# Kernel tuning notes

Measured on AMD Instinct MI355X. Metric: run time of the kernel, lower is better.

## Reference

```python
import jax, jax.numpy as jnp
import numpy as np

SLIDING_WINDOW = 512  # matches init kwarg
BLOCK_STRIDE = 32     # tokens per cache page


def setup_inputs() -> dict:
    key = jax.random.key(0)
    k0, k1, k2, k3 = jax.random.split(key, 4)
    B, S, HQ, HKV, D = 2, 2048, 32, 8, 128
    nb = S // BLOCK_STRIDE
    q = jax.random.normal(k0, (B, S, HQ, D), jnp.float32)
    k = jax.random.normal(k1, (B, S, HKV, D), jnp.float32)
    v = jax.random.normal(k2, (B, S, HKV, D), jnp.float32)
    sink = jax.random.normal(k3, (HQ,), jnp.float32)
    cache_state = jnp.zeros((B * nb, 2, HKV, BLOCK_STRIDE, D), jnp.float32)
    seq_block_ids = jnp.arange(B * nb, dtype=jnp.int32).reshape(B, nb)
    return {"q": q, "k": k, "v": v, "cache_state": cache_state,
            "seq_block_ids": seq_block_ids, "sink": sink}


def reference(q, k, v, cache_state, seq_block_ids, sink):
    B, S, HQ, D = q.shape
    HKV = k.shape[2]
    G = HQ // HKV  # GQA group size
    stride = cache_state.shape[3]
    nb = S // stride

    # --- write prefill K/V into the paged cache ---
    # pages laid out [num_pages, k/v, HKV, stride, D]
    k_pg = k.reshape(B, nb, stride, HKV, D).transpose(0, 1, 3, 2, 4).reshape(B * nb, HKV, stride, D)
    v_pg = v.reshape(B, nb, stride, HKV, D).transpose(0, 1, 3, 2, 4).reshape(B * nb, HKV, stride, D)
    ids = seq_block_ids.reshape(-1)
    new_cache = cache_state.at[ids, 0].set(k_pg).at[ids, 1].set(v_pg)

    # --- sliding-window causal attention with sink logits (GQA, no repeat) ---
    scale = 1.0 / np.sqrt(D).astype(np.float32)
    qg = q.reshape(B, S, HKV, G, D)
    # scores: [B, HKV, G, Sq, Sk]
    scores = jnp.einsum('bqhgd,bshd->bhgqs', qg, k) * scale
    i = jnp.arange(S)[:, None]
    j = jnp.arange(S)[None, :]
    allowed = (j <= i) & ((i - j) < SLIDING_WINDOW)  # causal banded mask
    neg = jnp.finfo(scores.dtype).min
    scores = jnp.where(allowed, scores, neg)
    # per-head sink logit appended as extra key column, dropped after softmax
    sink_col = jnp.broadcast_to(sink.reshape(HKV, G)[None, :, :, None, None], (B, HKV, G, S, 1))
    probs = jax.nn.softmax(jnp.concatenate([scores, sink_col], axis=-1), axis=-1)[..., :S]
    out = jnp.einsum('bhgqs,bshd->bqhgd', probs, v).reshape(B, S, HQ, D)
    return out, new_cache
```

## Files before the change

kernel.cpp:

```cpp
#include <hip/hip_runtime.h>
#include <hip/hip_bf16.h>
#include <stdint.h>

#define BB 2
#define SS 2048
#define HQ 32
#define HKV 8
#define DD 128
#define WIN 512

typedef __bf16 bf16x8 __attribute__((ext_vector_type(8)));
typedef float f32x16 __attribute__((ext_vector_type(16)));

__device__ __forceinline__ bf16x8 cvt8(float4 a, float4 b, float s) {
  bf16x8 r;
  r[0] = (__bf16)(a.x * s); r[1] = (__bf16)(a.y * s);
  r[2] = (__bf16)(a.z * s); r[3] = (__bf16)(a.w * s);
  r[4] = (__bf16)(b.x * s); r[5] = (__bf16)(b.y * s);
  r[6] = (__bf16)(b.z * s); r[7] = (__bf16)(b.w * s);
  return r;
}

__device__ __forceinline__ uint32_t pk2(float lo, float hi) {
  uint32_t w;
  asm("v_cvt_pk_bf16_f32 %0, %1, %2" : "=v"(w) : "v"(lo), "v"(hi));
  return w;
}

__global__ __launch_bounds__(512, 2) void attn_kernel(
    const float* __restrict__ qg, const float* __restrict__ kg,
    const float* __restrict__ vg, const float* __restrict__ sinkg,
    float* __restrict__ outg)
{
  const int col = (blockIdx.x & 7) + 8 * ((blockIdx.x >> 3) & 1);
  const int rank = blockIdx.x >> 4;
  const int qtile = rank < 24 ? rank + 8 : 31 - rank;
  const int hkv = col & 7, b = col >> 3;
  const int qb = qtile * 64;
  const int tid = threadIdx.x;
  const int wave = tid >> 6, lane = tid & 63;
  const int c5 = lane & 31, hi = lane >> 5;
  const int hq = (hkv << 2) + (wave >> 1);
  const int qw = qb + (wave & 1) * 32;
  const int qrow = qw + c5;

  __shared__ __align__(16) __bf16 Kl[2][64 * 128];
  __shared__ __align__(16) __bf16 Vt[2][128 * 64];

  const float LOG2E = 1.4426950408889634f;
  const float scale = 0.08838834764831845f * LOG2E;
  const float THR = 12.0f;

  bf16x8 qf[8];
  {
    const float* qp = qg + (((size_t)b * SS + qrow) * HQ + hq) * DD + hi * 8;
    #pragma unroll
    for (int ch = 0; ch < 8; ++ch) {
      float4 a = *(const float4*)(qp + ch * 16);
      float4 a2 = *(const float4*)(qp + ch * 16 + 4);
      qf[ch] = cvt8(a, a2, scale);
    }
  }
  const float sk = sinkg[hq] * LOG2E;

  float mm = -1e30f, ll = 0.f;
  f32x16 acc[4];
  #pragma unroll
  for (int d = 0; d < 4; ++d)
    #pragma unroll
    for (int r = 0; r < 16; ++r) acc[d][r] = 0.f;

  const int t0 = (qb > (WIN - 1) ? (qb - (WIN - 1)) : 0) >> 6;
  const int t1 = (qb + 63) >> 6;

  const int krow = tid >> 3, kchunk = tid & 7;
  const int vd = tid & 127, vslot = tid >> 7;
  const size_t KSTEP = (size_t)64 * HKV * DD;
  const float* kBase = kg + (((size_t)b * SS + krow) * HKV + hkv) * DD + kchunk * 16;
  const float* vBase = vg + (((size_t)b * SS + vslot * 16) * HKV + hkv) * DD + vd;

  float4 k0, k1, k2, k3; float vr[16];
  auto issue = [&](int t) {
    const float* kp = kBase + (size_t)t * KSTEP;
    k0 = *(const float4*)(kp);     k1 = *(const float4*)(kp + 4);
    k2 = *(const float4*)(kp + 8); k3 = *(const float4*)(kp + 12);
    const float* vp = vBase + (size_t)t * KSTEP;
    #pragma unroll
    for (int j = 0; j < 16; ++j) vr[j] = vp[(size_t)j * (HKV * DD)];
  };
  const int ksw = ((krow ^ (krow >> 3)) & 7) << 4;
  const int vsw = ((vd ^ (vd >> 3)) & 7) << 4;
  auto commit = [&](int buf) {
    char* kd = (char*)(&Kl[buf][0]) + krow * 256;
    *(bf16x8*)(kd + ((kchunk * 32) ^ ksw)) = cvt8(k0, k1, 1.f);
    *(bf16x8*)(kd + ((kchunk * 32 + 16) ^ ksw)) = cvt8(k2, k3, 1.f);
    char* vdst = (char*)(&Vt[buf][0]) + vd * 128;
    bf16x8 w0, w1;
    #pragma unroll
    for (int j = 0; j < 8; ++j) { w0[j] = (__bf16)vr[j]; w1[j] = (__bf16)vr[8 + j]; }
    *(bf16x8*)(vdst + ((vslot * 32) ^ vsw)) = w0;
    *(bf16x8*)(vdst + ((vslot * 32 + 16) ^ vsw)) = w1;
  };

  issue(t0);
  commit(0);
  __syncthreads();
  int cur = 0;

  const int swA = ((c5 ^ (c5 >> 3)) & 7) << 4;
  const int swB = swA ^ 0x40;

  for (int t = t0; t <= t1; ++t) {
    if (t < t1) issue(t + 1);
    const int kb = t << 6;
    const char* Ksc = (const char*)&Kl[cur][0];
    const char* Vsc = (const char*)&Vt[cur][0];

    f32x16 s0, s1;
    #pragma unroll
    for (int r = 0; r < 16; ++r) { s0[r] = 0.f; s1[r] = 0.f; }
    __builtin_amdgcn_s_setprio(1);
    #pragma unroll
    for (int ch = 0; ch < 8; ++ch) {
      const int colb = ch * 32 + hi * 16;
      bf16x8 a0 = *(const bf16x8*)(Ksc + c5 * 256 + (colb ^ swA));
      bf16x8 a1 = *(const bf16x8*)(Ksc + (32 + c5) * 256 + (colb ^ swB));
      s0 = __builtin_amdgcn_mfma_f32_32x32x16_bf16(a0, qf[ch], s0, 0, 0, 0);
      s1 = __builtin_amdgcn_mfma_f32_32x32x16_bf16(a1, qf[ch], s1, 0, 0, 0);
    }
    __builtin_amdgcn_s_setprio(0);

    const bool noMask = (kb + 63 <= qw) && (kb >= qw - (WIN - 32));

    if (!noMask) {
      #pragma unroll
      for (int r = 0; r < 16; ++r) {
        const int lr = (r & 3) + 8 * (r >> 2) + 4 * hi;
        const int kv0 = kb + lr, kv1 = kv0 + 32;
        const bool ok0 = (kv0 <= qrow) && (qrow - kv0 < WIN);
        const bool ok1 = (kv1 <= qrow) && (qrow - kv1 < WIN);
        s0[r] = ok0 ? s0[r] : -1e30f;
        s1[r] = ok1 ? s1[r] : -1e30f;
      }
    }
    float tmax = s0[0];
    #pragma unroll
    for (int r = 1; r < 16; ++r) tmax = fmaxf(tmax, s0[r]);
    #pragma unroll
    for (int r = 0; r < 16; ++r) tmax = fmaxf(tmax, s1[r]);
    tmax = fmaxf(tmax, __shfl_xor(tmax, 32));

    const bool resc = __any(tmax > mm + THR);
    const float mnew = resc ? fmaxf(mm, tmax) : mm;
    float tsum = 0.f;
    if (noMask) {
      #pragma unroll
      for (int r = 0; r < 16; ++r) {
        s0[r] = exp2f(s0[r] - mnew); tsum += s0[r];
        s1[r] = exp2f(s1[r] - mnew); tsum += s1[r];
      }
    } else {
      #pragma unroll
      for (int r = 0; r < 16; ++r) {
        s0[r] = (s0[r] > -9e29f) ? exp2f(s0[r] - mnew) : 0.f; tsum += s0[r];
        s1[r] = (s1[r] > -9e29f) ? exp2f(s1[r] - mnew) : 0.f; tsum += s1[r];
      }
    }
    tsum += __shfl_xor(tsum, 32);

    if (resc) {
      const float scl = exp2f(mm - mnew);
      ll = ll * scl + tsum;
      #pragma unroll
      for (int d = 0; d < 4; ++d)
        #pragma unroll
        for (int r = 0; r < 16; ++r) acc[d][r] *= scl;
      mm = mnew;
    } else {
      ll += tsum;
    }

    bf16x8 pb[4];
    #pragma unroll
    for (int kvq = 0; kvq < 4; ++kvq) {
      const int bq = (kvq & 1) * 8;
      float e0, e1, e2, e3, e4, e5, e6, e7;
      if (kvq & 2) {
        e0 = s1[bq+0]; e1 = s1[bq+1]; e2 = s1[bq+2]; e3 = s1[bq+3];
        e4 = s1[bq+4]; e5 = s1[bq+5]; e6 = s1[bq+6]; e7 = s1[bq+7];
      } else {
        e0 = s0[bq+0]; e1 = s0[bq+1]; e2 = s0[bq+2]; e3 = s0[bq+3];
        e4 = s0[bq+4]; e5 = s0[bq+5]; e6 = s0[bq+6]; e7 = s0[bq+7];
      }
      const uint32_t A0 = pk2(e0, e1), A1 = pk2(e2, e3);
      const uint32_t B0 = pk2(e4, e5), B1 = pk2(e6, e7);
      const uint32_t XA0 = __shfl_xor(A0, 32), XA1 = __shfl_xor(A1, 32);
      const uint32_t XB0 = __shfl_xor(B0, 32), XB1 = __shfl_xor(B1, 32);
      union { uint4 u; bf16x8 v; } cvu;
      cvu.u.x = hi ? XB0 : A0;
      cvu.u.y = hi ? XB1 : A1;
      cvu.u.z = hi ? B0 : XA0;
      cvu.u.w = hi ? B1 : XA1;
      pb[kvq] = cvu.v;
    }

    __builtin_amdgcn_s_setprio(1);
    #pragma unroll
    for (int d = 0; d < 4; ++d) {
      const int rowb = (d * 32 + c5) * 128;
      const int swV = swA ^ ((d & 1) << 6);
      #pragma unroll
      for (int kvq = 0; kvq < 4; ++kvq) {
        bf16x8 va = *(const bf16x8*)(Vsc + rowb + ((kvq * 32 + hi * 16) ^ swV));
        acc[d] = __builtin_amdgcn_mfma_f32_32x32x16_bf16(va, pb[kvq], acc[d], 0, 0, 0);
      }
    }
    __builtin_amdgcn_s_setprio(0);

    if (t < t1) {
      commit(cur ^ 1);
      __syncthreads();
      cur ^= 1;
    }
  }

  {
    const float Mf = fmaxf(mm, sk);
    const float ex = exp2f(mm - Mf);
    const float denom = ll * ex + exp2f(sk - Mf);
    const float fac = ex / denom;
    float* orow = outg + (((size_t)b * SS + qrow) * HQ + hq) * DD;
    #pragma unroll
    for (int d = 0; d < 4; ++d) {
      #pragma unroll
      for (int q4 = 0; q4 < 4; ++q4) {
        float4 o;
        o.x = acc[d][q4 * 4 + 0] * fac;
        o.y = acc[d][q4 * 4 + 1] * fac;
        o.z = acc[d][q4 * 4 + 2] * fac;
        o.w = acc[d][q4 * 4 + 3] * fac;
        *(float4*)(orow + d * 32 + q4 * 8 + 4 * hi) = o;
      }
    }
  }
}

__global__ void build_inv(const int* __restrict__ ids, int* __restrict__ inv,
                          int npages, int nslots) {
  const int i = threadIdx.x;
  if (i < npages) inv[i] = -1;
  __syncthreads();
  if (i < nslots) inv[ids[i]] = i;
}

__global__ void page_fill(const float* __restrict__ kg, const float* __restrict__ vg,
                          const float* __restrict__ cache_in, const int* __restrict__ inv,
                          float* __restrict__ cache) {
  const int page = blockIdx.x, half = blockIdx.y;
  const int slot = inv[page];
  float4* d4 = (float4*)cache;
  const size_t dbase = (((size_t)page * 2 + half) * 8) * 1024;
  if (slot >= 0) {
    const int b = slot >> 6, blk = slot & 63;
    const float4* s4 = (const float4*)(half ? vg : kg);
    for (int f = threadIdx.x; f < 8192; f += blockDim.x) {
      const int d = f & 31, s = (f >> 5) & 31, h = f >> 10;
      d4[dbase + (size_t)h * 1024 + s * 32 + d] =
          s4[(((size_t)b * SS + blk * 32 + s) * 8 + h) * 32 + d];
    }
  } else {
    const float4* s4 = (const float4*)cache_in;
    for (int f = threadIdx.x; f < 8192; f += blockDim.x)
      d4[dbase + f] = s4[dbase + f];
  }
}

__global__ void cache_copy(const float* __restrict__ src, float* __restrict__ dst, int n4) {
  const float4* s = (const float4*)src;
  float4* d = (float4*)dst;
  for (int i = blockIdx.x * blockDim.x + threadIdx.x; i < n4; i += gridDim.x * blockDim.x)
    d[i] = s[i];
}
__global__ void cache_scatter(const float* __restrict__ kg, const float* __restrict__ vg,
                              const int* __restrict__ ids, float* __restrict__ cache) {
  const int slot = blockIdx.x;
  const int half = blockIdx.y;
  const int b = slot >> 6, blk = slot & 63;
  const int page = ids[slot];
  const float4* s4 = (const float4*)(half ? vg : kg);
  float4* d4 = (float4*)cache;
  for (int f = threadIdx.x; f < 8192; f += blockDim.x) {
    const int d = f & 31, s = (f >> 5) & 31, h = f >> 10;
    d4[(((size_t)page * 2 + half) * 8 + h) * 1024 + s * 32 + d] =
        s4[(((size_t)b * SS + blk * 32 + s) * 8 + h) * 32 + d];
  }
}

extern "C" void kernel_launch(void* const* d_in, const int* in_sizes, int n_in,
                              void* d_out, int out_size, void* d_ws, size_t ws_size,
                              hipStream_t stream) {
  const float* q = (const float*)d_in[0];
  const float* k = (const float*)d_in[1];
  const float* v = (const float*)d_in[2];
  const float* cache_in = (const float*)d_in[3];
  const int* ids = (const int*)d_in[4];
  const float* sink = (const float*)d_in[5];
  float* out = (float*)d_out;
  float* cache_out = out + (size_t)BB * SS * HQ * DD;

  const int nslots = in_sizes[4];
  const int npages = in_sizes[3] / (2 * HKV * 32 * DD);

  if (ws_size >= (size_t)npages * sizeof(int) && npages <= 1024) {
    int* inv = (int*)d_ws;
    build_inv<<<1, 1024, 0, stream>>>(ids, inv, npages, nslots);
    page_fill<<<dim3(npages, 2), 256, 0, stream>>>(k, v, cache_in, inv, cache_out);
  } else {
    cache_copy<<<4096, 256, 0, stream>>>(cache_in, cache_out, (BB * SS * HKV * DD * 2) / 4);
    cache_scatter<<<dim3(BB * 64, 2), 256, 0, stream>>>(k, v, ids, cache_out);
  }
  attn_kernel<<<512, 512, 0, stream>>>(q, k, v, sink, out);
}
```

Baseline: 108.4 us.

## Precast K/V to bf16 with transposed V in workspace before attention

Adds a prep kernel that converts K to bf16 and writes a per-tile transposed bf16 V into workspace. The attention kernel then loads tiles with contiguous 16-byte vector loads and copies them straight into shared memory, replacing the strided fp32 loads and per-element conversion inside its pipelined loop. It also skips QK/PV work for 64-key tiles that lie entirely outside a wave's 32-row window. The cost is an extra kernel launch plus an extra read and write of all of K and V; the old path stays as a fallback when workspace is too small.

```diff
diff --git a/kernel.cpp b/kernel.cpp
--- a/kernel.cpp
+++ b/kernel.cpp
@@ -27,7 +27,262 @@
   return w;
 }
 
+__device__ __forceinline__ unsigned short bfu(float x) {
+  union { __bf16 b; unsigned short u; } c; c.b = (__bf16)x; return c.u;
+}
+
+#define SWZ(r) ((((r) ^ ((r) >> 3)) & 7) << 4)
+
 __global__ __launch_bounds__(512, 2) void attn_kernel(
+    const float* __restrict__ qg, const float* __restrict__ sinkg,
+    float* __restrict__ outg,
+    const unsigned short* __restrict__ kbg, const unsigned short* __restrict__ vtg)
+{
+  const int col = (blockIdx.x & 7) + 8 * ((blockIdx.x >> 3) & 1);
+  const int rank = blockIdx.x >> 4;
+  const int qtile = rank < 24 ? rank + 8 : 31 - rank;
+  const int hkv = col & 7, b = col >> 3;
+  const int qb = qtile * 64;
+  const int tid = threadIdx.x;
+  const int wave = tid >> 6, lane = tid & 63;
+  const int c5 = lane & 31, hi = lane >> 5;
+  const int hq = (hkv << 2) + (wave >> 1);
+  const int qw = qb + (wave & 1) * 32;
+  const int qrow = qw + c5;
+
+  __shared__ __align__(16) __bf16 Kl[2][64 * 128];
+  __shared__ __align__(16) __bf16 Vt[2][128 * 64];
+
+  const float LOG2E = 1.4426950408889634f;
+  const float scale = 0.08838834764831845f * LOG2E;
+  const float THR = 12.0f;
+
+  bf16x8 qf[8];
+  {
+    const float* qp = qg + (((size_t)b * SS + qrow) * HQ + hq) * DD + hi * 8;
+    #pragma unroll
+    for (int ch = 0; ch < 8; ++ch) {
+      float4 a = *(const float4*)(qp + ch * 16);
+      float4 a2 = *(const float4*)(qp + ch * 16 + 4);
+      qf[ch] = cvt8(a, a2, scale);
+    }
+  }
+  const float sk = sinkg[hq] * LOG2E;
+
+  float mm = -1e30f, ll = 0.f;
+  f32x16 acc[4];
+  #pragma unroll
+  for (int d = 0; d < 4; ++d)
+    #pragma unroll
+    for (int r = 0; r < 16; ++r) acc[d][r] = 0.f;
+
+  const int t0 = (qb > (WIN - 1) ? (qb - (WIN - 1)) : 0) >> 6;
+  const int t1 = (qb + 63) >> 6;
+
+  const char* kcol = (const char*)kbg + (size_t)(b * HKV + hkv) * (SS * DD * 2);
+  const char* vcol = (const char*)vtg + (size_t)(b * HKV + hkv) * (SS * DD * 2);
+  const int p0 = tid * 32;
+  const int kr = p0 >> 8, kx = p0 & 255;
+  const int vrw = p0 >> 7, vx = p0 & 127;
+  const int kd0 = kr * 256 + (kx ^ SWZ(kr)), kd1 = kr * 256 + ((kx + 16) ^ SWZ(kr));
+  const int vd0 = vrw * 128 + (vx ^ SWZ(vrw)), vd1 = vrw * 128 + ((vx + 16) ^ SWZ(vrw));
+
+  uint4 ksA, ksB, vsA, vsB;
+  auto issue = [&](int t) {
+    const char* kt = kcol + (size_t)t * 16384;
+    const char* vt = vcol + (size_t)t * 16384;
+    ksA = *(const uint4*)(kt + p0); ksB = *(const uint4*)(kt + p0 + 16);
+    vsA = *(const uint4*)(vt + p0); vsB = *(const uint4*)(vt + p0 + 16);
+  };
+  auto commit = [&](int buf) {
+    char* kb_ = (char*)&Kl[buf][0]; char* vb_ = (char*)&Vt[buf][0];
+    *(uint4*)(kb_ + kd0) = ksA; *(uint4*)(kb_ + kd1) = ksB;
+    *(uint4*)(vb_ + vd0) = vsA; *(uint4*)(vb_ + vd1) = vsB;
+  };
+
+  issue(t0);
+  commit(0);
+  __syncthreads();
+  int cur = 0;
+
+  const int swA = SWZ(c5);
+  const int swB = swA ^ 0x40;
+
+  for (int t = t0; t <= t1; ++t) {
+    if (t < t1) issue(t + 1);
+    const int kb = t << 6;
+
+    if (kb <= qw + 31 && kb + 63 >= qw - (WIN - 1)) {
+      const char* Ksc = (const char*)&Kl[cur][0];
+      const char* Vsc = (const char*)&Vt[cur][0];
+
+      f32x16 s0, s1;
+      #pragma unroll
+      for (int r = 0; r < 16; ++r) { s0[r] = 0.f; s1[r] = 0.f; }
+      __builtin_amdgcn_s_setprio(1);
+      #pragma unroll
+      for (int ch = 0; ch < 8; ++ch) {
+        const int colb = ch * 32 + hi * 16;
+        bf16x8 a0 = *(const bf16x8*)(Ksc + c5 * 256 + (colb ^ swA));
+        bf16x8 a1 = *(const bf16x8*)(Ksc + (32 + c5) * 256 + (colb ^ swB));
+        s0 = __builtin_amdgcn_mfma_f32_32x32x16_bf16(a0, qf[ch], s0, 0, 0, 0);
+        s1 = __builtin_amdgcn_mfma_f32_32x32x16_bf16(a1, qf[ch], s1, 0, 0, 0);
+      }
+      __builtin_amdgcn_s_setprio(0);
+
+      const bool noMask = (kb + 63 <= qw) && (kb >= qw - (WIN - 32));
+
+      if (!noMask) {
+        #pragma unroll
+        for (int r = 0; r < 16; ++r) {
+          const int lr = (r & 3) + 8 * (r >> 2) + 4 * hi;
+          const int kv0 = kb + lr, kv1 = kv0 + 32;
+          const bool ok0 = (kv0 <= qrow) && (qrow - kv0 < WIN);
+          const bool ok1 = (kv1 <= qrow) && (qrow - kv1 < WIN);
+          s0[r] = ok0 ? s0[r] : -1e30f;
+          s1[r] = ok1 ? s1[r] : -1e30f;
+        }
+      }
+      float tmax = s0[0];
+      #pragma unroll
+      for (int r = 1; r < 16; ++r) tmax = fmaxf(tmax, s0[r]);
+      #pragma unroll
+      for (int r = 0; r < 16; ++r) tmax = fmaxf(tmax, s1[r]);
+      tmax = fmaxf(tmax, __shfl_xor(tmax, 32));
+
+      const bool resc = __any(tmax > mm + THR);
+      const float mnew = resc ? fmaxf(mm, tmax) : mm;
+      float tsum = 0.f;
+      if (noMask) {
+        #pragma unroll
+        for (int r = 0; r < 16; ++r) {
+          s0[r] = exp2f(s0[r] - mnew); tsum += s0[r];
+          s1[r] = exp2f(s1[r] - mnew); tsum += s1[r];
+        }
+      } else {
+        #pragma unroll
+        for (int r = 0; r < 16; ++r) {
+          s0[r] = (s0[r] > -9e29f) ? exp2f(s0[r] - mnew) : 0.f; tsum += s0[r];
+          s1[r] = (s1[r] > -9e29f) ? exp2f(s1[r] - mnew) : 0.f; tsum += s1[r];
+        }
+      }
+      tsum += __shfl_xor(tsum, 32);
+
+      if (resc) {
+        const float scl = exp2f(mm - mnew);
+        ll = ll * scl + tsum;
+        #pragma unroll
+        for (int d = 0; d < 4; ++d)
+          #pragma unroll
+          for (int r = 0; r < 16; ++r) acc[d][r] *= scl;
+        mm = mnew;
+      } else {
+        ll += tsum;
+      }
+
+      bf16x8 pb[4];
+      #pragma unroll
+      for (int kvq = 0; kvq < 4; ++kvq) {
+        const int bq = (kvq & 1) * 8;
+        float e0, e1, e2, e3, e4, e5, e6, e7;
+        if (kvq & 2) {
+          e0 = s1[bq+0]; e1 = s1[bq+1]; e2 = s1[bq+2]; e3 = s1[bq+3];
+          e4 = s1[bq+4]; e5 = s1[bq+5]; e6 = s1[bq+6]; e7 = s1[bq+7];
+        } else {
+          e0 = s0[bq+0]; e1 = s0[bq+1]; e2 = s0[bq+2]; e3 = s0[bq+3];
+          e4 = s0[bq+4]; e5 = s0[bq+5]; e6 = s0[bq+6]; e7 = s0[bq+7];
+        }
+        const uint32_t A0 = pk2(e0, e1), A1 = pk2(e2, e3);
+        const uint32_t B0 = pk2(e4, e5), B1 = pk2(e6, e7);
+        const uint32_t XA0 = __shfl_xor(A0, 32), XA1 = __shfl_xor(A1, 32);
+        const uint32_t XB0 = __shfl_xor(B0, 32), XB1 = __shfl_xor(B1, 32);
+        union { uint4 u; bf16x8 v; } cvu;
+        cvu.u.x = hi ? XB0 : A0;
+        cvu.u.y = hi ? XB1 : A1;
+        cvu.u.z = hi ? B0 : XA0;
+        cvu.u.w = hi ? B1 : XA1;
+        pb[kvq] = cvu.v;
+      }
+
+      __builtin_amdgcn_s_setprio(1);
+      #pragma unroll
+      for (int d = 0; d < 4; ++d) {
+        const int rowb = (d * 32 + c5) * 128;
+        const int swV = swA ^ ((d & 1) << 6);
+        #pragma unroll
+        for (int kvq = 0; kvq < 4; ++kvq) {
+          bf16x8 va = *(const bf16x8*)(Vsc + rowb + ((kvq * 32 + hi * 16) ^ swV));
+          acc[d] = __builtin_amdgcn_mfma_f32_32x32x16_bf16(va, pb[kvq], acc[d], 0, 0, 0);
+        }
+      }
+      __builtin_amdgcn_s_setprio(0);
+    }
+
+    if (t < t1) {
+      commit(cur ^ 1);
+      __syncthreads();
+      cur ^= 1;
+    }
+  }
+
+  {
+    const float Mf = fmaxf(mm, sk);
+    const float ex = exp2f(mm - Mf);
+    const float denom = ll * ex + exp2f(sk - Mf);
+    const float fac = ex / denom;
+    float* orow = outg + (((size_t)b * SS + qrow) * HQ + hq) * DD;
+    #pragma unroll
+    for (int d = 0; d < 4; ++d) {
+      #pragma unroll
+      for (int q4 = 0; q4 < 4; ++q4) {
+        float4 o;
+        o.x = acc[d][q4 * 4 + 0] * fac;
+        o.y = acc[d][q4 * 4 + 1] * fac;
+        o.z = acc[d][q4 * 4 + 2] * fac;
+        o.w = acc[d][q4 * 4 + 3] * fac;
+        *(float4*)(orow + d * 32 + q4 * 8 + 4 * hi) = o;
+      }
+    }
+  }
+}
+
+__global__ void prep_kv(const float* __restrict__ kg, const float* __restrict__ vg,
+                        unsigned short* __restrict__ kb, unsigned short* __restrict__ vt) {
+  const int bx = blockIdx.x;
+  const int t = bx & 31, colx = bx >> 5;
+  const int b = colx >> 3, hkv = colx & 7;
+  const int kbrow = t * 64;
+  if (blockIdx.y == 0) {
+    #pragma unroll
+    for (int i = 0; i < 8; ++i) {
+      const int idx = i * 1024 + threadIdx.x * 4;
+      const int r = idx >> 7, d = idx & 127;
+      float4 v = *(const float4*)(kg + (((size_t)b * SS + kbrow + r) * HKV + hkv) * DD + d);
+      ushort4 o = make_ushort4(bfu(v.x), bfu(v.y), bfu(v.z), bfu(v.w));
+      *(ushort4*)(kb + ((size_t)colx * SS + kbrow + r) * DD + d) = o;
+    }
+  } else {
+    __shared__ unsigned short Vl[64][132];
+    #pragma unroll
+    for (int i = 0; i < 8; ++i) {
+      const int idx = i * 1024 + threadIdx.x * 4;
+      const int kv = idx >> 7, d = idx & 127;
+      float4 v = *(const float4*)(vg + (((size_t)b * SS + kbrow + kv) * HKV + hkv) * DD + d);
+      Vl[kv][d + 0] = bfu(v.x); Vl[kv][d + 1] = bfu(v.y);
+      Vl[kv][d + 2] = bfu(v.z); Vl[kv][d + 3] = bfu(v.w);
+    }
+    __syncthreads();
+    #pragma unroll
+    for (int i = 0; i < 8; ++i) {
+      const int idx = i * 1024 + threadIdx.x * 4;
+      const int d = idx >> 6, kv = idx & 63;
+      ushort4 o = make_ushort4(Vl[kv + 0][d], Vl[kv + 1][d], Vl[kv + 2][d], Vl[kv + 3][d]);
+      *(ushort4*)(vt + ((size_t)colx * 32 + t) * 8192 + d * 64 + kv) = o;
+    }
+  }
+}
+
+__global__ __launch_bounds__(512, 2) void attn_fallback(
     const float* __restrict__ qg, const float* __restrict__ kg,
     const float* __restrict__ vg, const float* __restrict__ sinkg,
     float* __restrict__ outg)
@@ -88,8 +343,8 @@
     #pragma unroll
     for (int j = 0; j < 16; ++j) vr[j] = vp[(size_t)j * (HKV * DD)];
   };
-  const int ksw = ((krow ^ (krow >> 3)) & 7) << 4;
-  const int vsw = ((vd ^ (vd >> 3)) & 7) << 4;
+  const int ksw = SWZ(krow);
+  const int vsw = SWZ(vd);
   auto commit = [&](int buf) {
     char* kd = (char*)(&Kl[buf][0]) + krow * 256;
     *(bf16x8*)(kd + ((kchunk * 32) ^ ksw)) = cvt8(k0, k1, 1.f);
@@ -107,123 +362,117 @@
   __syncthreads();
   int cur = 0;
 
-  const int swA = ((c5 ^ (c5 >> 3)) & 7) << 4;
+  const int swA = SWZ(c5);
   const int swB = swA ^ 0x40;
 
   for (int t = t0; t <= t1; ++t) {
     if (t < t1) issue(t + 1);
     const int kb = t << 6;
-    const char* Ksc = (const char*)&Kl[cur][0];
-    const char* Vsc = (const char*)&Vt[cur][0];
-
-    f32x16 s0, s1;
-    #pragma unroll
-    for (int r = 0; r < 16; ++r) { s0[r] = 0.f; s1[r] = 0.f; }
-    __builtin_amdgcn_s_setprio(1);
-    #pragma unroll
-    for (int ch = 0; ch < 8; ++ch) {
-      const int colb = ch * 32 + hi * 16;
-      bf16x8 a0 = *(const bf16x8*)(Ksc + c5 * 256 + (colb ^ swA));
-      bf16x8 a1 = *(const bf16x8*)(Ksc + (32 + c5) * 256 + (colb ^ swB));
-      s0 = __builtin_amdgcn_mfma_f32_32x32x16_bf16(a0, qf[ch], s0, 0, 0, 0);
-      s1 = __builtin_amdgcn_mfma_f32_32x32x16_bf16(a1, qf[ch], s1, 0, 0, 0);
-    }
-    __builtin_amdgcn_s_setprio(0);
-
-    const bool noMask = (kb + 63 <= qw) && (kb >= qw - (WIN - 32));
-
-    if (!noMask) {
-      #pragma unroll
-      for (int r = 0; r < 16; ++r) {
-        const int lr = (r & 3) + 8 * (r >> 2) + 4 * hi;
-        const int kv0 = kb + lr, kv1 = kv0 + 32;
-        const bool ok0 = (kv0 <= qrow) && (qrow - kv0 < WIN);
-        const bool ok1 = (kv1 <= qrow) && (qrow - kv1 < WIN);
-        s0[r] = ok0 ? s0[r] : -1e30f;
-        s1[r] = ok1 ? s1[r] : -1e30f;
-      }
-    }
-    float tmax = s0[0];
-    #pragma unroll
-    for (int r = 1; r < 16; ++r) tmax = fmaxf(tmax, s0[r]);
-    #pragma unroll
-    for (int r = 0; r < 16; ++r) tmax = fmaxf(tmax, s1[r]);
-    tmax = fmaxf(tmax, __shfl_xor(tmax, 32));
-
-    const bool resc = __any(tmax > mm + THR);
-    const float mnew = resc ? fmaxf(mm, tmax) : mm;
-    float tsum = 0.f;
-    if (noMask) {
-      #pragma unroll
-      for (int r = 0; r < 16; ++r) {
-        s0[r] = exp2f(s0[r] - mnew); tsum += s0[r];
-        s1[r] = exp2f(s1[r] - mnew); tsum += s1[r];
-      }
-    } else {
-      #pragma unroll
-      for (int r = 0; r < 16; ++r) {
-        s0[r] = (s0[r] > -9e29f) ? exp2f(s0[r] - mnew) : 0.f; tsum += s0[r];
-        s1[r] = (s1[r] > -9e29f) ? exp2f(s1[r] - mnew) : 0.f; tsum += s1[r];
-      }
-    }
-    tsum += __shfl_xor(tsum, 32);
-
-    if (resc) {
-      const float scl = exp2f(mm - mnew);
-      ll = ll * scl + tsum;
-      #pragma unroll
-      for (int d = 0; d < 4; ++d)
-        #pragma unroll
-        for (int r = 0; r < 16; ++r) acc[d][r] *= scl;
-      mm = mnew;
-    } else {
-      ll += tsum;
-    }
-
-    bf16x8 pb[4];
-    #pragma unroll
-    for (int kvq = 0; kvq < 4; ++kvq) {
-      const int bq = (kvq & 1) * 8;
-      float e0, e1, e2, e3, e4, e5, e6, e7;
-      if (kvq & 2) {
-        e0 = s1[bq+0]; e1 = s1[bq+1]; e2 = s1[bq+2]; e3 = s1[bq+3];
-        e4 = s1[bq+4]; e5 = s1[bq+5]; e6 = s1[bq+6]; e7 = s1[bq+7];
+    if (kb <= qw + 31 && kb + 63 >= qw - (WIN - 1)) {
+      const char* Ksc = (const char*)&Kl[cur][0];
+      const char* Vsc = (const char*)&Vt[cur][0];
+      f32x16 s0, s1;
+      #pragma unroll
+      for (int r = 0; r < 16; ++r) { s0[r] = 0.f; s1[r] = 0.f; }
+      __builtin_amdgcn_s_setprio(1);
+      #pragma unroll
+      for (int ch = 0; ch < 8; ++ch) {
+        const int colb = ch * 32 + hi * 16;
+        bf16x8 a0 = *(const bf16x8*)(Ksc + c5 * 256 + (colb ^ swA));
+        bf16x8 a1 = *(const bf16x8*)(Ksc + (32 + c5) * 256 + (colb ^ swB));
+        s0 = __builtin_amdgcn_mfma_f32_32x32x16_bf16(a0, qf[ch], s0, 0, 0, 0);
+        s1 = __builtin_amdgcn_mfma_f32_32x32x16_bf16(a1, qf[ch], s1, 0, 0, 0);
+      }
+      __builtin_amdgcn_s_setprio(0);
+
+      const bool noMask = (kb + 63 <= qw) && (kb >= qw - (WIN - 32));
+      if (!noMask) {
+        #pragma unroll
+        for (int r = 0; r < 16; ++r) {
+          const int lr = (r & 3) + 8 * (r >> 2) + 4 * hi;
+          const int kv0 = kb + lr, kv1 = kv0 + 32;
+          const bool ok0 = (kv0 <= qrow) && (qrow - kv0 < WIN);
+          const bool ok1 = (kv1 <= qrow) && (qrow - kv1 < WIN);
+          s0[r] = ok0 ? s0[r] : -1e30f;
+          s1[r] = ok1 ? s1[r] : -1e30f;
+        }
+      }
+      float tmax = s0[0];
+      #pragma unroll
+      for (int r = 1; r < 16; ++r) tmax = fmaxf(tmax, s0[r]);
+      #pragma unroll
+      for (int r = 0; r < 16; ++r) tmax = fmaxf(tmax, s1[r]);
+      tmax = fmaxf(tmax, __shfl_xor(tmax, 32));
+      const bool resc = __any(tmax > mm + THR);
+      const float mnew = resc ? fmaxf(mm, tmax) : mm;
+      float tsum = 0.f;
+      if (noMask) {
+        #pragma unroll
+        for (int r = 0; r < 16; ++r) {
+          s0[r] = exp2f(s0[r] - mnew); tsum += s0[r];
+          s1[r] = exp2f(s1[r] - mnew); tsum += s1[r];
+        }
       } else {
-        e0 = s0[bq+0]; e1 = s0[bq+1]; e2 = s0[bq+2]; e3 = s0[bq+3];
-        e4 = s0[bq+4]; e5 = s0[bq+5]; e6 = s0[bq+6]; e7 = s0[bq+7];
-      }
-      const uint32_t A0 = pk2(e0, e1), A1 = pk2(e2, e3);
-      const uint32_t B0 = pk2(e4, e5), B1 = pk2(e6, e7);
-      const uint32_t XA0 = __shfl_xor(A0, 32), XA1 = __shfl_xor(A1, 32);
-      const uint32_t XB0 = __shfl_xor(B0, 32), XB1 = __shfl_xor(B1, 32);
-      union { uint4 u; bf16x8 v; } cvu;
-      cvu.u.x = hi ? XB0 : A0;
-      cvu.u.y = hi ? XB1 : A1;
-      cvu.u.z = hi ? B0 : XA0;
-      cvu.u.w = hi ? B1 : XA1;
-      pb[kvq] = cvu.v;
-    }
-
-    __builtin_amdgcn_s_setprio(1);
-    #pragma unroll
-    for (int d = 0; d < 4; ++d) {
-      const int rowb = (d * 32 + c5) * 128;
-      const int swV = swA ^ ((d & 1) << 6);
+        #pragma unroll
+        for (int r = 0; r < 16; ++r) {
+          s0[r] = (s0[r] > -9e29f) ? exp2f(s0[r] - mnew) : 0.f; tsum += s0[r];
+          s1[r] = (s1[r] > -9e29f) ? exp2f(s1[r] - mnew) : 0.f; tsum += s1[r];
+        }
+      }
+      tsum += __shfl_xor(tsum, 32);
+      if (resc) {
+        const float scl = exp2f(mm - mnew);
+        ll = ll * scl + tsum;
+        #pragma unroll
+        for (int d = 0; d < 4; ++d)
+          #pragma unroll
+          for (int r = 0; r < 16; ++r) acc[d][r] *= scl;
+        mm = mnew;
+      } else {
+        ll += tsum;
+      }
+      bf16x8 pb[4];
       #pragma unroll
       for (int kvq = 0; kvq < 4; ++kvq) {
-        bf16x8 va = *(const bf16x8*)(Vsc + rowb + ((kvq * 32 + hi * 16) ^ swV));
-        acc[d] = __builtin_amdgcn_mfma_f32_32x32x16_bf16(va, pb[kvq], acc[d], 0, 0, 0);
-      }
-    }
-    __builtin_amdgcn_s_setprio(0);
-
+        const int bq = (kvq & 1) * 8;
+        float e0, e1, e2, e3, e4, e5, e6, e7;
+        if (kvq & 2) {
+          e0 = s1[bq+0]; e1 = s1[bq+1]; e2 = s1[bq+2]; e3 = s1[bq+3];
+          e4 = s1[bq+4]; e5 = s1[bq+5]; e6 = s1[bq+6]; e7 = s1[bq+7];
+        } else {
+          e0 = s0[bq+0]; e1 = s0[bq+1]; e2 = s0[bq+2]; e3 = s0[bq+3];
+          e4 = s0[bq+4]; e5 = s0[bq+5]; e6 = s0[bq+6]; e7 = s0[bq+7];
+        }
+        const uint32_t A0 = pk2(e0, e1), A1 = pk2(e2, e3);
+        const uint32_t B0 = pk2(e4, e5), B1 = pk2(e6, e7);
+        const uint32_t XA0 = __shfl_xor(A0, 32), XA1 = __shfl_xor(A1, 32);
+        const uint32_t XB0 = __shfl_xor(B0, 32), XB1 = __shfl_xor(B1, 32);
+        union { uint4 u; bf16x8 v; } cvu;
+        cvu.u.x = hi ? XB0 : A0;
+        cvu.u.y = hi ? XB1 : A1;
+        cvu.u.z = hi ? B0 : XA0;
+        cvu.u.w = hi ? B1 : XA1;
+        pb[kvq] = cvu.v;
+      }
+      __builtin_amdgcn_s_setprio(1);
+      #pragma unroll
+      for (int d = 0; d < 4; ++d) {
+        const int rowb = (d * 32 + c5) * 128;
+        const int swV = swA ^ ((d & 1) << 6);
+        #pragma unroll
+        for (int kvq = 0; kvq < 4; ++kvq) {
+          bf16x8 va = *(const bf16x8*)(Vsc + rowb + ((kvq * 32 + hi * 16) ^ swV));
+          acc[d] = __builtin_amdgcn_mfma_f32_32x32x16_bf16(va, pb[kvq], acc[d], 0, 0, 0);
+        }
+      }
+      __builtin_amdgcn_s_setprio(0);
+    }
     if (t < t1) {
       commit(cur ^ 1);
       __syncthreads();
       cur ^= 1;
     }
   }
-
   {
     const float Mf = fmaxf(mm, sk);
     const float ex = exp2f(mm - Mf);
@@ -311,13 +560,26 @@
   const int nslots = in_sizes[4];
   const int npages = in_sizes[3] / (2 * HKV * 32 * DD);
 
-  if (ws_size >= (size_t)npages * sizeof(int) && npages <= 1024) {
+  const size_t kvBytes = (size_t)BB * HKV * SS * DD * 2;
+  const size_t need = 4096 + 2 * kvBytes;
+  const bool smallMaps = (npages <= 1024) && (nslots <= 1024);
+
+  if (ws_size >= need && smallMaps) {
+    int* inv = (int*)d_ws;
+    unsigned short* kbp = (unsigned short*)((char*)d_ws + 4096);
+    unsigned short* vtp = kbp + kvBytes / 2;
+    build_inv<<<1, 1024, 0, stream>>>(ids, inv, npages, nslots);
+    page_fill<<<dim3(npages, 2), 256, 0, stream>>>(k, v, cache_in, inv, cache_out);
+    prep_kv<<<dim3(BB * HKV * 32, 2), 256, 0, stream>>>(k, v, kbp, vtp);
+    attn_kernel<<<512, 512, 0, stream>>>(q, sink, out, kbp, vtp);
+  } else if (ws_size >= (size_t)npages * sizeof(int) && smallMaps) {
     int* inv = (int*)d_ws;
     build_inv<<<1, 1024, 0, stream>>>(ids, inv, npages, nslots);
     page_fill<<<dim3(npages, 2), 256, 0, stream>>>(k, v, cache_in, inv, cache_out);
+    attn_fallback<<<512, 512, 0, stream>>>(q, k, v, sink, out);
   } else {
     cache_copy<<<4096, 256, 0, stream>>>(cache_in, cache_out, (BB * SS * HKV * DD * 2) / 4);
     cache_scatter<<<dim3(BB * 64, 2), 256, 0, stream>>>(k, v, ids, cache_out);
-  }
-  attn_kernel<<<512, 512, 0, stream>>>(q, k, v, sink, out);
-}
+    attn_fallback<<<512, 512, 0, stream>>>(q, k, v, sink, out);
+  }
+}
```

Measured after the change: 107.8 us. No clear change (-0.5%).
